# Kernel tuning notes

Measured on AMD Instinct MI355X. Metric: run time of the kernel, lower is better.

## Reference

```python
import jax, jax.numpy as jnp
import numpy as np


def setup_inputs() -> dict:
    key = jax.random.key(0)
    VOCAB = 50257
    BATCH, SEQ = 512, 8192
    assignments = jax.random.randint(key, (BATCH, SEQ), 0, VOCAB, dtype=jnp.int64 if jax.config.jax_enable_x64 else jnp.int32)
    return {"assignments": assignments, "vocab_size": VOCAB}


def reference(assignments, vocab_size):
    # Faithful math: counts[b, v] = sum_t (assignments[b, t] == v), then
    # frequency = counts / counts.sum(-1, keepdim=True).
    # Implemented as a per-row scatter-add histogram (same result, no O(N*V*S) blowup).
    def _hist(row):  # row: [seq] int -> [vocab] float32
        return jnp.zeros((vocab_size,), dtype=jnp.float32).at[row].add(1.0)

    counts = jax.vmap(_hist)(assignments)  # [batch, vocab]
    frequency = counts / counts.sum(axis=-1, keepdims=True)
    return frequency
```

## Files before the change

kernel.cpp:

```cpp
#include <hip/hip_runtime.h>


#define TF_BLOCK 256
#define TF_CHUNK 12800
#define TF_NCHUNK 4
#define TF_VPT 32

__global__ __launch_bounds__(TF_BLOCK)
void XTermFrequency_hist_kernel(const int* __restrict__ assign,
                                float* __restrict__ out,
                                int V, int S, float scale) {
    __shared__ unsigned int hist[TF_CHUNK];
    const int row = blockIdx.x;
    const int tid = threadIdx.x;

    const int4* rowp = (const int4*)(assign + (long long)row * S);
    int4 vals[TF_VPT / 4];
#pragma unroll
    for (int k = 0; k < TF_VPT / 4; ++k) {
        vals[k] = rowp[tid + k * TF_BLOCK];
    }

    float* __restrict__ orow = out + (long long)row * V;

    for (int c = 0; c < TF_NCHUNK; ++c) {
        const int base = c * TF_CHUNK;
        const int len = min(V - base, TF_CHUNK);

        for (int i = tid; i < TF_CHUNK; i += TF_BLOCK) hist[i] = 0u;
        __syncthreads();

#pragma unroll
        for (int k = 0; k < TF_VPT / 4; ++k) {
            const int4 v4 = vals[k];
            unsigned int d;
            d = (unsigned int)(v4.x - base);
            if (d < (unsigned int)TF_CHUNK) atomicAdd(&hist[d], 1u);
            d = (unsigned int)(v4.y - base);
            if (d < (unsigned int)TF_CHUNK) atomicAdd(&hist[d], 1u);
            d = (unsigned int)(v4.z - base);
            if (d < (unsigned int)TF_CHUNK) atomicAdd(&hist[d], 1u);
            d = (unsigned int)(v4.w - base);
            if (d < (unsigned int)TF_CHUNK) atomicAdd(&hist[d], 1u);
        }
        __syncthreads();

        for (int i = tid; i < len; i += TF_BLOCK) {
            orow[base + i] = (float)hist[i] * scale;
        }
        __syncthreads();
    }
}

extern "C" void kernel_launch(void* const* d_in, const int* in_sizes, int n_in,
                              void* d_out, int out_size, void* d_ws, size_t ws_size,
                              hipStream_t stream) {
    const int* assign = (const int*)d_in[0];
    float* out = (float*)d_out;

    const int V = 50257;
    const int B = out_size / V;
    const int S = in_sizes[0] / B;
    const float scale = 1.0f / (float)S;

    XTermFrequency_hist_kernel<<<dim3(B), dim3(TF_BLOCK), 0, stream>>>(
        assign, out, V, S, scale);
}
```

Before: 118.9 us.

## Split each row's histogram across four blocks with packed 16-bit shared counters

Each block now handles one vocab chunk of one row, so the grid grows to four times the batch size and every block reads the row's assignments once. Pairs of 16-bit counters are packed into 32-bit shared words, which halves LDS per block so more blocks fit on a CU, and launch bounds ask for six waves per SIMD. Output is written with nontemporal stores. The cost is reading the input four times from memory or cache. Packed counters would overflow if a row's sequence length were 65536 or more.

```diff
diff --git a/kernel.cpp b/kernel.cpp
--- a/kernel.cpp
+++ b/kernel.cpp
@@ -3,16 +3,21 @@
 
 #define TF_BLOCK 256
 #define TF_CHUNK 12800
+#define TF_WORDS (TF_CHUNK / 2)
 #define TF_NCHUNK 4
 #define TF_VPT 32
 
-__global__ __launch_bounds__(TF_BLOCK)
+__global__ __launch_bounds__(TF_BLOCK, 6)
 void XTermFrequency_hist_kernel(const int* __restrict__ assign,
                                 float* __restrict__ out,
                                 int V, int S, float scale) {
-    __shared__ unsigned int hist[TF_CHUNK];
-    const int row = blockIdx.x;
+    __shared__ unsigned int hist[TF_WORDS];
+    const int bid = blockIdx.x;
+    const int row = bid >> 2;
+    const int c   = bid & 3;
     const int tid = threadIdx.x;
+    const int base = c * TF_CHUNK;
+    const int len  = min(V - base, TF_CHUNK);
 
     const int4* rowp = (const int4*)(assign + (long long)row * S);
     int4 vals[TF_VPT / 4];
@@ -21,34 +26,33 @@
         vals[k] = rowp[tid + k * TF_BLOCK];
     }
 
-    float* __restrict__ orow = out + (long long)row * V;
-
-    for (int c = 0; c < TF_NCHUNK; ++c) {
-        const int base = c * TF_CHUNK;
-        const int len = min(V - base, TF_CHUNK);
-
-        for (int i = tid; i < TF_CHUNK; i += TF_BLOCK) hist[i] = 0u;
-        __syncthreads();
+#pragma unroll
+    for (int i = 0; i < TF_WORDS / TF_BLOCK; ++i) {
+        hist[tid + i * TF_BLOCK] = 0u;
+    }
+    __syncthreads();
 
 #pragma unroll
-        for (int k = 0; k < TF_VPT / 4; ++k) {
-            const int4 v4 = vals[k];
-            unsigned int d;
-            d = (unsigned int)(v4.x - base);
-            if (d < (unsigned int)TF_CHUNK) atomicAdd(&hist[d], 1u);
-            d = (unsigned int)(v4.y - base);
-            if (d < (unsigned int)TF_CHUNK) atomicAdd(&hist[d], 1u);
-            d = (unsigned int)(v4.z - base);
-            if (d < (unsigned int)TF_CHUNK) atomicAdd(&hist[d], 1u);
-            d = (unsigned int)(v4.w - base);
-            if (d < (unsigned int)TF_CHUNK) atomicAdd(&hist[d], 1u);
-        }
-        __syncthreads();
+    for (int k = 0; k < TF_VPT / 4; ++k) {
+        const int4 v4 = vals[k];
+        unsigned int d;
+        d = (unsigned int)(v4.x - base);
+        if (d < (unsigned int)TF_CHUNK) atomicAdd(&hist[d >> 1], 1u << ((d & 1u) << 4));
+        d = (unsigned int)(v4.y - base);
+        if (d < (unsigned int)TF_CHUNK) atomicAdd(&hist[d >> 1], 1u << ((d & 1u) << 4));
+        d = (unsigned int)(v4.z - base);
+        if (d < (unsigned int)TF_CHUNK) atomicAdd(&hist[d >> 1], 1u << ((d & 1u) << 4));
+        d = (unsigned int)(v4.w - base);
+        if (d < (unsigned int)TF_CHUNK) atomicAdd(&hist[d >> 1], 1u << ((d & 1u) << 4));
+    }
+    __syncthreads();
 
-        for (int i = tid; i < len; i += TF_BLOCK) {
-            orow[base + i] = (float)hist[i] * scale;
-        }
-        __syncthreads();
+    float* __restrict__ orow = out + (long long)row * V + base;
+    const unsigned int sh = (tid & 1u) << 4;
+    for (int i = tid; i < len; i += TF_BLOCK) {
+        const unsigned int w = hist[i >> 1];
+        const float f = (float)((w >> sh) & 0xFFFFu) * scale;
+        __builtin_nontemporal_store(f, &orow[i]);
     }
 }
 
@@ -63,6 +67,6 @@
     const int S = in_sizes[0] / B;
     const float scale = 1.0f / (float)S;
 
-    XTermFrequency_hist_kernel<<<dim3(B), dim3(TF_BLOCK), 0, stream>>>(
+    XTermFrequency_hist_kernel<<<dim3(B * TF_NCHUNK), dim3(TF_BLOCK), 0, stream>>>(
         assign, out, V, S, scale);
 }
```

After: 137.6 us. +15.8%, slower.
